# Performance work log

Measured on AMD Instinct MI355X. Metric: run time of the kernel, lower is better.

The kernel has to match this reference:

```python
import jax, jax.numpy as jnp
import numpy as np

HEADS = 2
C1 = 33    # per-head out channels, conv1
C2 = 550   # per-head out channels, conv2


def _lin_params(key, fan_in, fan_out):
    kw, kb = jax.random.split(key)
    scale = 1.0 / np.sqrt(fan_in)
    W = jax.random.uniform(kw, (fan_in, fan_out), jnp.float32, -scale, scale)
    b = jax.random.uniform(kb, (fan_out,), jnp.float32, -scale, scale)
    return W, b


def transformer_conv(x, src, dst, Wq, bq, Wk, bk, Wv, bv, Ws, bs, heads, out_ch):
    """PyG TransformerConv (concat=True, root_weight=True, beta=False)."""
    N = x.shape[0]
    q = (x @ Wq + bq).reshape(N, heads, out_ch)  # query of target node i
    k = (x @ Wk + bk).reshape(N, heads, out_ch)  # key of source node j
    v = (x @ Wv + bv).reshape(N, heads, out_ch)  # value of source node j
    # attention logits per edge: [E, H]
    alpha = jnp.einsum('ehc,ehc->eh', q[dst], k[src]) / jnp.sqrt(jnp.float32(out_ch))
    # segment softmax over incoming edges of each dst node
    m = jax.lax.stop_gradient(jax.ops.segment_max(alpha, dst, num_segments=N))  # [N,H]
    e = jnp.exp(alpha - m[dst])
    denom = jax.ops.segment_sum(e, dst, num_segments=N)  # [N,H]
    a = e / denom[dst]
    # weighted scatter-aggregate of source values: [N,H,C]
    out = jax.ops.segment_sum(a[..., None] * v[src], dst, num_segments=N)
    out = out.reshape(N, heads * out_ch)
    # root/skip connection
    out = out + x @ Ws + bs
    return out


def setup_inputs() -> dict:
    key = jax.random.key(0)
    ks = jax.random.split(key, 10)
    N, E, IN = 20000, 120000, 256
    x = jax.random.normal(ks[0], (N, IN), jnp.float32)
    edge_index = jax.random.randint(ks[1], (2, E), 0, N, jnp.int64 if jax.config.jax_enable_x64 else jnp.int32)
    d = {'x': x, 'edge_index': edge_index}
    # conv1: IN -> heads*C1
    d['Wq1'], d['bq1'] = _lin_params(ks[2], IN, HEADS * C1)
    d['Wk1'], d['bk1'] = _lin_params(ks[3], IN, HEADS * C1)
    d['Wv1'], d['bv1'] = _lin_params(ks[4], IN, HEADS * C1)
    d['Ws1'], d['bs1'] = _lin_params(ks[5], IN, HEADS * C1)
    # conv2: heads*C1 -> heads*C2
    IN2 = HEADS * C1
    d['Wq2'], d['bq2'] = _lin_params(ks[6], IN2, HEADS * C2)
    d['Wk2'], d['bk2'] = _lin_params(ks[7], IN2, HEADS * C2)
    d['Wv2'], d['bv2'] = _lin_params(ks[8], IN2, HEADS * C2)
    d['Ws2'], d['bs2'] = _lin_params(ks[9], IN2, HEADS * C2)
    return d


def reference(x, edge_index, Wq1, bq1, Wk1, bk1, Wv1, bv1, Ws1, bs1,
              Wq2, bq2, Wk2, bk2, Wv2, bv2, Ws2, bs2):
    src, dst = edge_index[0], edge_index[1]
    h = transformer_conv(x, src, dst, Wq1, bq1, Wk1, bk1, Wv1, bv1, Ws1, bs1, HEADS, C1)
    h = transformer_conv(h, src, dst, Wq2, bq2, Wk2, bk2, Wv2, bv2, Ws2, bs2, HEADS, C2)
    # x.view(N, 550, heads).max(dim=2) -- faithful to the original reshape layout
    h = h.reshape(h.shape[0], C2, HEADS)
    return jnp.max(h, axis=2)
```

## Files before the change

### kernel.cpp

```cpp
#include <hip/hip_runtime.h>
#include <math.h>

#define HEADS 2
#define C1    33
#define C2    550
#define D1    66
#define D2    1100
#define IN1   256
#define PROJW 288
#define KU    224
#define N2P   1152
#define KZ    96
#define ZW    144

typedef __attribute__((ext_vector_type(8))) short bfrag;
typedef __attribute__((ext_vector_type(4))) float f32x4;

__device__ inline unsigned short f2bf(float f) {
    unsigned int u = __float_as_uint(f);
    u += 0x7FFFu + ((u >> 16) & 1u);
    return (unsigned short)(u >> 16);
}

__device__ inline int xcd_slot(int bid, int slots) {
    return (bid >> 3) + (bid & 7) * slots;
}

__global__ void k_cvt(const float* __restrict__ x, unsigned short* __restrict__ xb, int total4) {
    int i = blockIdx.x * blockDim.x + threadIdx.x;
    if (i >= total4) return;
    float4 v = ((const float4*)x)[i];
    ushort4 o;
    o.x = f2bf(v.x); o.y = f2bf(v.y); o.z = f2bf(v.z); o.w = f2bf(v.w);
    ((ushort4*)xb)[i] = o;
}

__global__ void k_prep1(const float* __restrict__ Wq, const float* __restrict__ bq,
                        const float* __restrict__ Wk, const float* __restrict__ bk,
                        const float* __restrict__ Wv, const float* __restrict__ bv,
                        const float* __restrict__ Ws, const float* __restrict__ bs,
                        unsigned short* __restrict__ Wt1, float* __restrict__ bcat) {
    int bid = blockIdx.x;
    int lk = bid & 3, t = bid >> 2;
    int ks = t & 7, g = t >> 3;
    int col = threadIdx.x;
    int c = g * 96 + col;
    int k0 = ks * 32 + lk * 8;
    short vals[8];
    float bia = 0.f;
    if (c < 4 * D1) {
        int m = c / D1, j = c % D1;
        const float* W; const float* B;
        switch (m) {
            case 0: W = Wq; B = bq; break;
            case 1: W = Wk; B = bk; break;
            case 2: W = Wv; B = bv; break;
            default: W = Ws; B = bs; break;
        }
        #pragma unroll
        for (int e = 0; e < 8; e++) vals[e] = (short)f2bf(W[(size_t)(k0 + e) * D1 + j]);
        bia = B[j];
    } else {
        #pragma unroll
        for (int e = 0; e < 8; e++) vals[e] = 0;
    }
    *(bfrag*)&Wt1[((size_t)bid * 96 + col) * 8] = *(bfrag*)vals;
    if (ks == 0 && lk == 0) bcat[c] = bia;
}

__global__ void k_prep2(const float* __restrict__ Wv2, const float* __restrict__ bv2,
                        const float* __restrict__ Ws2, const float* __restrict__ bs2,
                        unsigned short* __restrict__ W2t) {
    int bid = blockIdx.x;
    int lk = bid & 3, t = bid >> 2;
    int ks = t % 7, g = t / 7;
    int col = threadIdx.x;
    int c = g * 96 + col;
    int k0 = ks * 32 + lk * 8;
    short vals[8];
    #pragma unroll
    for (int e = 0; e < 8; e++) {
        int k = k0 + e;
        float val = 0.f;
        if (c < D2) {
            if (c < C2) {
                if (k < 66) val = Wv2[(size_t)k * D2 + c];
                else if (k >= 132 && k < 198) val = Ws2[(size_t)(k - 132) * D2 + c];
                else if (k == 198) val = bv2[c];
                else if (k == 223) val = bs2[c];
            } else {
                if (k >= 66 && k < 132) val = Wv2[(size_t)(k - 66) * D2 + c];
                else if (k >= 132 && k < 198) val = Ws2[(size_t)(k - 132) * D2 + c];
                else if (k == 199) val = bv2[c];
                else if (k == 223) val = bs2[c];
            }
        }
        vals[e] = (short)f2bf(val);
    }
    *(bfrag*)&W2t[((size_t)bid * 96 + col) * 8] = *(bfrag*)vals;
}

__global__ void k_hist(const int* __restrict__ dst, int E, int* __restrict__ cnt) {
    int e = blockIdx.x * blockDim.x + threadIdx.x;
    if (e < E) atomicAdd(&cnt[dst[e]], 1);
}

__global__ void k_scan(const int* __restrict__ cnt, int* __restrict__ roff,
                       int* __restrict__ pos, int N) {
    __shared__ int wsum[16];
    __shared__ int carry_s;
    int tid = threadIdx.x, wid = tid >> 6, lane = tid & 63;
    if (tid == 0) { carry_s = 0; roff[0] = 0; }
    __syncthreads();
    for (int base = 0; base < N; base += 1024) {
        int i = base + tid;
        int v = (i < N) ? cnt[i] : 0;
        int x = v;
        #pragma unroll
        for (int s = 1; s < 64; s <<= 1) {
            int t = __shfl_up(x, s, 64);
            if (lane >= s) x += t;
        }
        if (lane == 63) wsum[wid] = x;
        __syncthreads();
        if (tid < 16) {
            int y = wsum[tid];
            #pragma unroll
            for (int s = 1; s < 16; s <<= 1) {
                int t = __shfl_up(y, s, 16);
                if (tid >= s) y += t;
            }
            wsum[tid] = y;
        }
        __syncthreads();
        int carry = carry_s;
        int incl = carry + (wid ? wsum[wid - 1] : 0) + x;
        if (i < N) { roff[i + 1] = incl; pos[i] = incl - v; }
        __syncthreads();
        if (tid == 0) carry_s = carry + wsum[15];
        __syncthreads();
    }
}

__global__ void k_fill(const int* __restrict__ src, const int* __restrict__ dst, int E,
                       int* __restrict__ pos, int* __restrict__ elist) {
    int e = blockIdx.x * blockDim.x + threadIdx.x;
    if (e < E) {
        int slot = atomicAdd(&pos[dst[e]], 1);
        elist[slot] = src[e];
    }
}

__global__ __launch_bounds__(256) void k_mm1(
        const unsigned short* __restrict__ A, const unsigned short* __restrict__ B,
        const float* __restrict__ bias, float* __restrict__ proj, int N,
        int nRow, int slots) {
    int s = xcd_slot(blockIdx.x, slots);
    if (s >= nRow * 3) return;
    int rowt = s / 3, g = s - rowt * 3;
    int cbase = g * 96;
    int wave = threadIdx.x >> 6, lane = threadIdx.x & 63;
    int lr = lane & 15, lk = lane >> 4;
    int rbase = rowt * 128 + wave * 32;
    int ar[2];
    #pragma unroll
    for (int mi = 0; mi < 2; mi++) {
        int r = rbase + mi * 16 + lr;
        ar[mi] = (r < N) ? r : (N - 1);
    }
    bfrag a[2][8];
    #pragma unroll
    for (int mi = 0; mi < 2; mi++)
        #pragma unroll
        for (int ks = 0; ks < 8; ks++)
            a[mi][ks] = *(const bfrag*)(A + (size_t)ar[mi] * IN1 + ks * 32 + lk * 8);
    f32x4 acc[2][6];
    #pragma unroll
    for (int mi = 0; mi < 2; mi++)
        #pragma unroll
        for (int ni = 0; ni < 6; ni++) acc[mi][ni] = (f32x4){0.f, 0.f, 0.f, 0.f};
    #pragma unroll
    for (int ks = 0; ks < 8; ks++) {
        bfrag b[6];
        #pragma unroll
        for (int ni = 0; ni < 6; ni++)
            b[ni] = *(const bfrag*)(B + (size_t)(g * 8 + ks) * 3072 + lk * 768 + (ni * 16 + lr) * 8);
        #pragma unroll
        for (int mi = 0; mi < 2; mi++)
            #pragma unroll
            for (int ni = 0; ni < 6; ni++)
                acc[mi][ni] = __builtin_amdgcn_mfma_f32_16x16x32_bf16(a[mi][ks], b[ni], acc[mi][ni], 0, 0, 0);
    }
    #pragma unroll
    for (int mi = 0; mi < 2; mi++) {
        #pragma unroll
        for (int ni = 0; ni < 6; ni++) {
            int col = cbase + ni * 16 + lr;
            float bia = bias[col];
            #pragma unroll
            for (int r = 0; r < 4; r++) {
                int row = rbase + mi * 16 + lk * 4 + r;
                if (row < N) proj[(size_t)row * PROJW + col] = acc[mi][ni][r] + bia;
            }
        }
    }
}

__global__ __launch_bounds__(128) void k_conv1(
        const float* __restrict__ proj, const int* __restrict__ roff,
        const int* __restrict__ elist, float* __restrict__ h1,
        unsigned short* __restrict__ h1b, int N) {
    int n = blockIdx.x;
    int h = threadIdx.x >> 6;
    int lane = threadIdx.x & 63;
    int half = lane >> 5, l32 = lane & 31;
    size_t pb = (size_t)n * PROJW;
    int hc = h * C1;
    float q_a = proj[pb + hc + l32];
    float q_b = (l32 == 0) ? proj[pb + hc + 32] : 0.f;
    int E0 = roff[n], E1 = roff[n + 1];
    float m = -INFINITY, lsum = 0.f, aca = 0.f, acb = 0.f;
    const float isc = 0.17407765595569785f;
    int i = E0 + half;
    for (; i + 2 < E1; i += 4) {
        int s0 = elist[i], s1 = elist[i + 2];
        size_t b0 = (size_t)s0 * PROJW, b1 = (size_t)s1 * PROJW;
        float k0a = proj[b0 + 66 + hc + l32];
        float k0b = (l32 == 0) ? proj[b0 + 66 + hc + 32] : 0.f;
        float k1a = proj[b1 + 66 + hc + l32];
        float k1b = (l32 == 0) ? proj[b1 + 66 + hc + 32] : 0.f;
        float v0a = proj[b0 + 132 + hc + l32];
        float v0b = (l32 == 0) ? proj[b0 + 132 + hc + 32] : 0.f;
        float v1a = proj[b1 + 132 + hc + l32];
        float v1b = (l32 == 0) ? proj[b1 + 132 + hc + 32] : 0.f;
        float p0 = q_a * k0a + q_b * k0b;
        float p1 = q_a * k1a + q_b * k1b;
        #pragma unroll
        for (int off = 16; off >= 1; off >>= 1) {
            p0 += __shfl_xor(p0, off, 32);
            p1 += __shfl_xor(p1, off, 32);
        }
        float a0 = p0 * isc, a1 = p1 * isc;
        float mp = fmaxf(a0, a1);
        float e0 = __expf(a0 - mp), e1 = __expf(a1 - mp);
        float lp = e0 + e1;
        float apa = e0 * v0a + e1 * v1a;
        float apb = e0 * v0b + e1 * v1b;
        float mnew = fmaxf(m, mp);
        float sc = __expf(m - mnew), sp = __expf(mp - mnew);
        lsum = lsum * sc + lp * sp;
        aca = aca * sc + apa * sp;
        acb = acb * sc + apb * sp;
        m = mnew;
    }
    for (; i < E1; i += 2) {
        int s = elist[i];
        size_t sb = (size_t)s * PROJW;
        float ka = proj[sb + 66 + hc + l32];
        float kb = (l32 == 0) ? proj[sb + 66 + hc + 32] : 0.f;
        float va = proj[sb + 132 + hc + l32];
        float vb = (l32 == 0) ? proj[sb + 132 + hc + 32] : 0.f;
        float p = q_a * ka + q_b * kb;
        #pragma unroll
        for (int off = 16; off >= 1; off >>= 1) p += __shfl_xor(p, off, 32);
        float alpha = p * isc;
        float mnew = fmaxf(m, alpha);
        float sc = __expf(m - mnew);
        float pe = __expf(alpha - mnew);
        lsum = lsum * sc + pe;
        aca = aca * sc + pe * va;
        acb = acb * sc + pe * vb;
        m = mnew;
    }
    float mO  = __shfl_xor(m, 32, 64);
    float lO  = __shfl_xor(lsum, 32, 64);
    float aaO = __shfl_xor(aca, 32, 64);
    float abO = __shfl_xor(acb, 32, 64);
    float mnew = fmaxf(m, mO);
    float sS = (m  > -INFINITY) ? __expf(m  - mnew) : 0.f;
    float sO = (mO > -INFINITY) ? __expf(mO - mnew) : 0.f;
    lsum = lsum * sS + lO * sO;
    aca  = aca * sS + aaO * sO;
    acb  = acb * sS + abO * sO;
    float inv = (lsum > 0.f) ? 1.f / lsum : 0.f;
    if (half == 0) {
        float s1a = proj[pb + 198 + hc + l32];
        float val = aca * inv + s1a;
        h1[(size_t)n * D1 + hc + l32] = val;
        h1b[(size_t)n * KZ + hc + l32] = f2bf(val);
        if (l32 == 0) {
            float s1b = proj[pb + 198 + hc + 32];
            float valb = acb * inv + s1b;
            h1[(size_t)n * D1 + hc + 32] = valb;
            h1b[(size_t)n * KZ + hc + 32] = f2bf(valb);
        }
    } else if (h == 1 && l32 < 30) {
        h1b[(size_t)n * KZ + D1 + l32] = 0;
    }
}

__global__ __launch_bounds__(256) void k_precomp(
        const float* __restrict__ Wq2, const float* __restrict__ bq2,
        const float* __restrict__ Wk2, const float* __restrict__ bk2,
        float* __restrict__ G, float* __restrict__ wqbk,
        float* __restrict__ wkbq, float* __restrict__ cc) {
    int wave = threadIdx.x >> 6, lane = threadIdx.x & 63;
    int j = blockIdx.x * 4 + wave;
    if (j >= 8978) return;
    const float *u, *v;
    float* outp;
    if (j < 8976) {
        int h = j / 4488;
        int r = j % 4488;
        int a = r / 68, b = r % 68;
        if (b < 66)      { u = Wq2 + (size_t)a * D2 + h * C2; v = Wk2 + (size_t)b * D2 + h * C2; outp = &G[h * 4356 + a * 66 + b]; }
        else if (b == 66){ u = Wq2 + (size_t)a * D2 + h * C2; v = bk2 + h * C2;                  outp = &wqbk[h * 66 + a]; }
        else             { u = Wk2 + (size_t)a * D2 + h * C2; v = bq2 + h * C2;                  outp = &wkbq[h * 66 + a]; }
    } else {
        int h = j - 8976;
        u = bq2 + h * C2; v = bk2 + h * C2; outp = &cc[h];
    }
    float acc = 0.f;
    for (int c = lane; c < C2; c += 64) acc += u[c] * v[c];
    #pragma unroll
    for (int off = 32; off >= 1; off >>= 1) acc += __shfl_xor(acc, off, 64);
    if (lane == 0) *outp = acc;
}

__global__ void k_prepz(const float* __restrict__ G, const float* __restrict__ wqbk,
                        const float* __restrict__ wkbq, unsigned short* __restrict__ GBt) {
    int bid = blockIdx.x;
    int lk = bid & 3, t = bid >> 2;
    int ks = t % 3, g = t / 3;
    int col = threadIdx.x;
    int r = g * 96 + col;
    int k0 = ks * 32 + lk * 8;
    short vals[8];
    #pragma unroll
    for (int e = 0; e < 8; e++) {
        int k = k0 + e;
        float v = 0.f;
        if (k < D1) {
            if (r < 132) v = G[r * D1 + k];
            else if (r < 134) v = wqbk[(r - 132) * D1 + k];
            else if (r < 136) v = wkbq[(r - 134) * D1 + k];
        }
        vals[e] = (short)f2bf(v);
    }
    *(bfrag*)&GBt[((size_t)bid * 96 + col) * 8] = *(bfrag*)vals;
}

__global__ __launch_bounds__(256) void k_mmz(
        const unsigned short* __restrict__ A, const unsigned short* __restrict__ B,
        float* __restrict__ Z, int N, int nRow, int slots) {
    int s = xcd_slot(blockIdx.x, slots);
    if (s >= nRow * 2) return;
    int rowt = s >> 1, g = s & 1;
    int wave = threadIdx.x >> 6, lane = threadIdx.x & 63;
    int lr = lane & 15, lk = lane >> 4;
    int rbase = rowt * 64 + (wave >> 1) * 32;
    int ch = (wave & 1) * 48;
    int cbase = g * 96 + ch;
    f32x4 acc[2][3];
    #pragma unroll
    for (int i = 0; i < 2; i++)
        #pragma unroll
        for (int j = 0; j < 3; j++) acc[i][j] = (f32x4){0.f, 0.f, 0.f, 0.f};
    int ar[2];
    #pragma unroll
    for (int mi = 0; mi < 2; mi++) {
        int r = rbase + mi * 16 + lr;
        ar[mi] = (r < N) ? r : (N - 1);
    }
    #pragma unroll
    for (int ks = 0; ks < 3; ks++) {
        bfrag a[2], b[3];
        #pragma unroll
        for (int mi = 0; mi < 2; mi++)
            a[mi] = *(const bfrag*)(A + (size_t)ar[mi] * KZ + ks * 32 + lk * 8);
        #pragma unroll
        for (int ni = 0; ni < 3; ni++)
            b[ni] = *(const bfrag*)(B + (size_t)(g * 3 + ks) * 3072 + lk * 768 + (ch + ni * 16 + lr) * 8);
        #pragma unroll
        for (int mi = 0; mi < 2; mi++)
            #pragma unroll
            for (int ni = 0; ni < 3; ni++)
                acc[mi][ni] = __builtin_amdgcn_mfma_f32_16x16x32_bf16(a[mi], b[ni], acc[mi][ni], 0, 0, 0);
    }
    #pragma unroll
    for (int mi = 0; mi < 2; mi++) {
        #pragma unroll
        for (int ni = 0; ni < 3; ni++) {
            int col = cbase + ni * 16 + lr;
            if (col >= 136) continue;
            #pragma unroll
            for (int r = 0; r < 4; r++) {
                int row = rbase + mi * 16 + lk * 4 + r;
                if (row < N) Z[(size_t)row * ZW + col] = acc[mi][ni][r];
            }
        }
    }
}

__global__ __launch_bounds__(128) void k_conv2(
        const float* __restrict__ h1, const float* __restrict__ Z,
        const float* __restrict__ cc, const int* __restrict__ roff,
        const int* __restrict__ elist, unsigned short* __restrict__ U, int N) {
    int n = blockIdx.x;
    int h = threadIdx.x >> 6;
    int lane = threadIdx.x & 63;
    int half = lane >> 5, l32 = lane & 31;
    int hD = h * D1;
    size_t nb = (size_t)n * D1;
    float hd_a = h1[nb + l32];
    float hd_b = h1[nb + 32 + l32];
    float hd_c = (l32 < 2) ? h1[nb + 64 + l32] : 0.f;
    float adv = Z[(size_t)n * ZW + 132 + h] + cc[h];
    int E0 = roff[n], E1 = roff[n + 1];
    float m = -INFINITY, lsum = 0.f, aa = 0.f, ab = 0.f, ac = 0.f;
    const float isc = 0.04264014327112209f;
    int i = E0 + half;
    for (; i + 2 < E1; i += 4) {
        int s0 = elist[i], s1 = elist[i + 2];
        const float* z0 = Z + (size_t)s0 * ZW;
        const float* z1 = Z + (size_t)s1 * ZW;
        float z0c = (l32 < 2) ? z0[hD + 64 + l32] : 0.f;
        float z1c = (l32 < 2) ? z1[hD + 64 + l32] : 0.f;
        float p0 = hd_a * z0[hD + l32] + hd_b * z0[hD + 32 + l32] + hd_c * z0c;
        float p1 = hd_a * z1[hD + l32] + hd_b * z1[hD + 32 + l32] + hd_c * z1c;
        float as0 = z0[134 + h], as1 = z1[134 + h];
        #pragma unroll
        for (int off = 16; off >= 1; off >>= 1) {
            p0 += __shfl_xor(p0, off, 32);
            p1 += __shfl_xor(p1, off, 32);
        }
        float al0 = (p0 + adv + as0) * isc;
        float al1 = (p1 + adv + as1) * isc;
        size_t v0b = (size_t)s0 * D1, v1b = (size_t)s1 * D1;
        float v0a = h1[v0b + l32], v0bb = h1[v0b + 32 + l32];
        float v0c = (l32 < 2) ? h1[v0b + 64 + l32] : 0.f;
        float v1a = h1[v1b + l32], v1bb = h1[v1b + 32 + l32];
        float v1c = (l32 < 2) ? h1[v1b + 64 + l32] : 0.f;
        float mp = fmaxf(al0, al1);
        float e0 = __expf(al0 - mp), e1 = __expf(al1 - mp);
        float lp = e0 + e1;
        float mnew = fmaxf(m, mp);
        float sc = __expf(m - mnew), sp = __expf(mp - mnew);
        lsum = lsum * sc + lp * sp;
        aa = aa * sc + (e0 * v0a + e1 * v1a) * sp;
        ab = ab * sc + (e0 * v0bb + e1 * v1bb) * sp;
        ac = ac * sc + (e0 * v0c + e1 * v1c) * sp;
        m = mnew;
    }
    for (; i < E1; i += 2) {
        int s = elist[i];
        const float* zr = Z + (size_t)s * ZW;
        float zc = (l32 < 2) ? zr[hD + 64 + l32] : 0.f;
        float p = hd_a * zr[hD + l32] + hd_b * zr[hD + 32 + l32] + hd_c * zc;
        float as_ = zr[134 + h];
        #pragma unroll
        for (int off = 16; off >= 1; off >>= 1) p += __shfl_xor(p, off, 32);
        float alpha = (p + adv + as_) * isc;
        size_t vb = (size_t)s * D1;
        float va = h1[vb + l32], vbb = h1[vb + 32 + l32];
        float vc = (l32 < 2) ? h1[vb + 64 + l32] : 0.f;
        float mnew = fmaxf(m, alpha);
        float sc = __expf(m - mnew);
        float pe = __expf(alpha - mnew);
        lsum = lsum * sc + pe;
        aa = aa * sc + pe * va;
        ab = ab * sc + pe * vbb;
        ac = ac * sc + pe * vc;
        m = mnew;
    }
    float mO  = __shfl_xor(m, 32, 64);
    float lO  = __shfl_xor(lsum, 32, 64);
    float aaO = __shfl_xor(aa, 32, 64);
    float abO = __shfl_xor(ab, 32, 64);
    float acO = __shfl_xor(ac, 32, 64);
    float mnew = fmaxf(m, mO);
    float sS = (m  > -INFINITY) ? __expf(m  - mnew) : 0.f;
    float sO = (mO > -INFINITY) ? __expf(mO - mnew) : 0.f;
    lsum = lsum * sS + lO * sO;
    aa = aa * sS + aaO * sO;
    ab = ab * sS + abO * sO;
    ac = ac * sS + acO * sO;
    float inv = (lsum > 0.f) ? 1.f / lsum : 0.f;
    size_t ub = (size_t)n * KU;
    if (half == 0) {
        U[ub + hD + l32] = f2bf(aa * inv);
        if (l32 < 2) U[ub + hD + 64 + l32] = f2bf(ac * inv);
    } else {
        U[ub + hD + 32 + l32] = f2bf(ab * inv);
    }
    if (lane == 0) U[ub + 198 + h] = (lsum > 0.f) ? (unsigned short)0x3F80 : (unsigned short)0;
    if (h == 0) {
        if (half == 0) {
            U[ub + 132 + l32] = f2bf(hd_a);
            if (l32 < 2) U[ub + 132 + 64 + l32] = f2bf(hd_c);
            if (l32 == 2) U[ub + 223] = (unsigned short)0x3F80;
        } else {
            U[ub + 132 + 32 + l32] = f2bf(hd_b);
        }
    } else if (half == 1 && l32 < 23) {
        U[ub + 200 + l32] = 0;
    }
}

__global__ __launch_bounds__(256) void k_mm2(
        const unsigned short* __restrict__ A, const unsigned short* __restrict__ B,
        float* __restrict__ out, int N, int nRow, int slots) {
    __shared__ float ot[4][32][49];
    int s = xcd_slot(blockIdx.x, slots);
    if (s >= nRow * 12) return;
    int rowt = s / 12, g = s - rowt * 12;
    int wave = threadIdx.x >> 6, lane = threadIdx.x & 63;
    int lr = lane & 15, lk = lane >> 4;
    int rbase = rowt * 128 + wave * 32;
    int ar[2];
    #pragma unroll
    for (int mi = 0; mi < 2; mi++) {
        int r = rbase + mi * 16 + lr;
        ar[mi] = (r < N) ? r : (N - 1);
    }
    bfrag a[2][7];
    #pragma unroll
    for (int mi = 0; mi < 2; mi++)
        #pragma unroll
        for (int ks = 0; ks < 7; ks++)
            a[mi][ks] = *(const bfrag*)(A + (size_t)ar[mi] * KU + ks * 32 + lk * 8);
    f32x4 acc[2][6];
    #pragma unroll
    for (int mi = 0; mi < 2; mi++)
        #pragma unroll
        for (int ni = 0; ni < 6; ni++) acc[mi][ni] = (f32x4){0.f, 0.f, 0.f, 0.f};
    #pragma unroll
    for (int ks = 0; ks < 7; ks++) {
        bfrag b[6];
        #pragma unroll
        for (int ni = 0; ni < 6; ni++)
            b[ni] = *(const bfrag*)(B + (size_t)(g * 7 + ks) * 3072 + lk * 768 + (ni * 16 + lr) * 8);
        #pragma unroll
        for (int mi = 0; mi < 2; mi++)
            #pragma unroll
            for (int ni = 0; ni < 6; ni++)
                acc[mi][ni] = __builtin_amdgcn_mfma_f32_16x16x32_bf16(a[mi][ks], b[ni], acc[mi][ni], 0, 0, 0);
    }
    #pragma unroll
    for (int mi = 0; mi < 2; mi++) {
        #pragma unroll
        for (int ni = 0; ni < 6; ni++) {
            #pragma unroll
            for (int r = 0; r < 4; r++) {
                float val = acc[mi][ni][r];
                float oth = __shfl_xor(val, 1, 64);
                if (!(lane & 1))
                    ot[wave][mi * 16 + lk * 4 + r][ni * 8 + (lr >> 1)] = fmaxf(val, oth);
            }
        }
    }
    __syncthreads();
    int colb = g * 48;
    #pragma unroll
    for (int i = 0; i < 24; i++) {
        int t = i * 64 + lane;
        int r32 = t / 48, pos = t - r32 * 48;
        int row = rbase + r32;
        int col = colb + pos;
        if (row < N && col < C2)
            out[(size_t)row * C2 + col] = ot[wave][r32][pos];
    }
}

extern "C" void kernel_launch(void* const* d_in, const int* in_sizes, int n_in,
                              void* d_out, int out_size, void* d_ws, size_t ws_size,
                              hipStream_t stream) {
    const float* x  = (const float*)d_in[0];
    const int*   ei = (const int*)d_in[1];
    int N = in_sizes[0] / IN1;
    int E = in_sizes[1] / 2;
    const int* src = ei;
    const int* dst = ei + E;

    const float *Wq1 = (const float*)d_in[2],  *bq1 = (const float*)d_in[3];
    const float *Wk1 = (const float*)d_in[4],  *bk1 = (const float*)d_in[5];
    const float *Wv1 = (const float*)d_in[6],  *bv1 = (const float*)d_in[7];
    const float *Ws1 = (const float*)d_in[8],  *bs1 = (const float*)d_in[9];
    const float *Wq2 = (const float*)d_in[10], *bq2 = (const float*)d_in[11];
    const float *Wk2 = (const float*)d_in[12], *bk2 = (const float*)d_in[13];
    const float *Wv2 = (const float*)d_in[14], *bv2 = (const float*)d_in[15];
    const float *Ws2 = (const float*)d_in[16], *bs2 = (const float*)d_in[17];

    char* w = (char*)d_ws;
    size_t off = 0;
    auto take = [&](size_t bytes) { size_t o = off; off = (off + bytes + 255) & ~(size_t)255; return o; };

    unsigned short* xb = (unsigned short*)(w + take((size_t)N * IN1 * 2));
    size_t proj_off = take((size_t)N * PROJW * 4);
    float* proj = (float*)(w + proj_off);
    float* Z = proj;
    unsigned short* U = (unsigned short*)(w + proj_off + (size_t)N * ZW * 4);
    float* h1   = (float*)(w + take((size_t)N * D1 * 4));
    unsigned short* h1b = (unsigned short*)(w + take((size_t)N * KZ * 2));
    float* G    = (float*)(w + take((size_t)2 * D1 * D1 * 4));
    float* wqbk = (float*)(w + take(2 * D1 * 4));
    float* wkbq = (float*)(w + take(2 * D1 * 4));
    float* cc   = (float*)(w + take(2 * 4));
    unsigned short* GBt = (unsigned short*)(w + take((size_t)24 * 96 * 8 * 2));
    unsigned short* Wt1 = (unsigned short*)(w + take((size_t)96 * 96 * 8 * 2));
    float* bcat = (float*)(w + take(PROJW * 4));
    unsigned short* W2t = (unsigned short*)(w + take((size_t)336 * 96 * 8 * 2));
    int* cnt   = (int*)(w + take((size_t)N * 4));
    int* roff  = (int*)(w + take((size_t)(N + 1) * 4));
    int* pos   = (int*)(w + take((size_t)N * 4));
    int* elist = (int*)(w + take((size_t)E * 4));

    hipMemsetAsync(cnt, 0, (size_t)N * sizeof(int), stream);
    k_hist<<<(E + 255) / 256, 256, 0, stream>>>(dst, E, cnt);
    k_scan<<<1, 1024, 0, stream>>>(cnt, roff, pos, N);
    k_fill<<<(E + 255) / 256, 256, 0, stream>>>(src, dst, E, pos, elist);

    k_cvt<<<(N * IN1 / 4 + 255) / 256, 256, 0, stream>>>(x, xb, N * IN1 / 4);
    k_prep1<<<96, 96, 0, stream>>>(Wq1, bq1, Wk1, bk1, Wv1, bv1, Ws1, bs1, Wt1, bcat);
    k_prep2<<<336, 96, 0, stream>>>(Wv2, bv2, Ws2, bs2, W2t);
    k_precomp<<<(8978 + 3) / 4, 256, 0, stream>>>(Wq2, bq2, Wk2, bk2, G, wqbk, wkbq, cc);
    k_prepz<<<24, 96, 0, stream>>>(G, wqbk, wkbq, GBt);

    int nRow1 = (N + 127) / 128;
    int tot1  = nRow1 * 3;
    int slots1 = (tot1 + 7) / 8;
    int nRowZ = (N + 63) / 64;
    int totZ  = nRowZ * 2;
    int slotsZ = (totZ + 7) / 8;
    int nRow2 = (N + 127) / 128;
    int tot2  = nRow2 * 12;
    int slots2 = (tot2 + 7) / 8;

    k_mm1<<<slots1 * 8, 256, 0, stream>>>(xb, Wt1, bcat, proj, N, nRow1, slots1);
    k_conv1<<<N, 128, 0, stream>>>(proj, roff, elist, h1, h1b, N);

    k_mmz<<<slotsZ * 8, 256, 0, stream>>>(h1b, GBt, Z, N, nRowZ, slotsZ);

    k_conv2<<<N, 128, 0, stream>>>(h1, Z, cc, roff, elist, U, N);

    k_mm2<<<slots2 * 8, 256, 0, stream>>>(U, W2t, (float*)d_out, N, nRow2, slots2);
}
```

Before: 173.1 us.

## Store intermediates in bf16, fuse x conversion into mm1, merge precompute kernels

```diff
diff --git a/kernel.cpp b/kernel.cpp
--- a/kernel.cpp
+++ b/kernel.cpp
@@ -9,7 +9,6 @@
 #define IN1   256
 #define PROJW 288
 #define KU    224
-#define N2P   1152
 #define KZ    96
 #define ZW    144
 
@@ -21,18 +20,12 @@
     u += 0x7FFFu + ((u >> 16) & 1u);
     return (unsigned short)(u >> 16);
 }
+__device__ inline float bf2f(unsigned short u) {
+    return __uint_as_float((unsigned int)u << 16);
+}
 
 __device__ inline int xcd_slot(int bid, int slots) {
     return (bid >> 3) + (bid & 7) * slots;
-}
-
-__global__ void k_cvt(const float* __restrict__ x, unsigned short* __restrict__ xb, int total4) {
-    int i = blockIdx.x * blockDim.x + threadIdx.x;
-    if (i >= total4) return;
-    float4 v = ((const float4*)x)[i];
-    ushort4 o;
-    o.x = f2bf(v.x); o.y = f2bf(v.y); o.z = f2bf(v.z); o.w = f2bf(v.w);
-    ((ushort4*)xb)[i] = o;
 }
 
 __global__ void k_prep1(const float* __restrict__ Wq, const float* __restrict__ bq,
@@ -151,9 +144,48 @@
     }
 }
 
+__global__ __launch_bounds__(256) void k_precomp(
+        const float* __restrict__ Wq2, const float* __restrict__ bq2,
+        const float* __restrict__ Wk2, const float* __restrict__ bk2,
+        unsigned short* __restrict__ GBt, float* __restrict__ cc) {
+    int wave = threadIdx.x >> 6, lane = threadIdx.x & 63;
+    int j = blockIdx.x * 4 + wave;
+    if (j >= 8978) return;
+    const float *u, *v;
+    int h = 0, a = 0, b = 0;
+    if (j < 8976) {
+        h = j / 4488;
+        int r = j % 4488;
+        a = r / 68; b = r % 68;
+        if (b < 66)      { u = Wq2 + (size_t)a * D2 + h * C2; v = Wk2 + (size_t)b * D2 + h * C2; }
+        else if (b == 66){ u = Wq2 + (size_t)a * D2 + h * C2; v = bk2 + h * C2; }
+        else             { u = Wk2 + (size_t)a * D2 + h * C2; v = bq2 + h * C2; }
+    } else {
+        h = j - 8976;
+        u = bq2 + h * C2; v = bk2 + h * C2;
+    }
+    float acc = 0.f;
+    for (int c = lane; c < C2; c += 64) acc += u[c] * v[c];
+    #pragma unroll
+    for (int off = 32; off >= 1; off >>= 1) acc += __shfl_xor(acc, off, 64);
+    if (lane == 0) {
+        if (j < 8976) {
+            int r, k;
+            if (b < 66)      { r = h * 66 + a; k = b; }
+            else if (b == 66){ r = 132 + h;    k = a; }
+            else             { r = 134 + h;    k = a; }
+            int g = r / 96, cm = r % 96;
+            int ks2 = k >> 5, rem = k & 31, lk2 = rem >> 3, e = rem & 7;
+            GBt[(((size_t)(g * 3 + ks2) * 4 + lk2) * 96 + cm) * 8 + e] = f2bf(acc);
+        } else {
+            cc[h] = acc;
+        }
+    }
+}
+
 __global__ __launch_bounds__(256) void k_mm1(
-        const unsigned short* __restrict__ A, const unsigned short* __restrict__ B,
-        const float* __restrict__ bias, float* __restrict__ proj, int N,
+        const float* __restrict__ X, const unsigned short* __restrict__ B,
+        const float* __restrict__ bias, unsigned short* __restrict__ projb, int N,
         int nRow, int slots) {
     int s = xcd_slot(blockIdx.x, slots);
     if (s >= nRow * 3) return;
@@ -172,8 +204,17 @@
     #pragma unroll
     for (int mi = 0; mi < 2; mi++)
         #pragma unroll
-        for (int ks = 0; ks < 8; ks++)
-            a[mi][ks] = *(const bfrag*)(A + (size_t)ar[mi] * IN1 + ks * 32 + lk * 8);
+        for (int ks = 0; ks < 8; ks++) {
+            const float* p = X + (size_t)ar[mi] * IN1 + ks * 32 + lk * 8;
+            float4 v0 = *(const float4*)p;
+            float4 v1 = *(const float4*)(p + 4);
+            bfrag r;
+            r[0] = (short)f2bf(v0.x); r[1] = (short)f2bf(v0.y);
+            r[2] = (short)f2bf(v0.z); r[3] = (short)f2bf(v0.w);
+            r[4] = (short)f2bf(v1.x); r[5] = (short)f2bf(v1.y);
+            r[6] = (short)f2bf(v1.z); r[7] = (short)f2bf(v1.w);
+            a[mi][ks] = r;
+        }
     f32x4 acc[2][6];
     #pragma unroll
     for (int mi = 0; mi < 2; mi++)
@@ -200,24 +241,23 @@
             #pragma unroll
             for (int r = 0; r < 4; r++) {
                 int row = rbase + mi * 16 + lk * 4 + r;
-                if (row < N) proj[(size_t)row * PROJW + col] = acc[mi][ni][r] + bia;
+                if (row < N) projb[(size_t)row * PROJW + col] = f2bf(acc[mi][ni][r] + bia);
             }
         }
     }
 }
 
 __global__ __launch_bounds__(128) void k_conv1(
-        const float* __restrict__ proj, const int* __restrict__ roff,
-        const int* __restrict__ elist, float* __restrict__ h1,
-        unsigned short* __restrict__ h1b, int N) {
+        const unsigned short* __restrict__ projb, const int* __restrict__ roff,
+        const int* __restrict__ elist, unsigned short* __restrict__ h1b, int N) {
     int n = blockIdx.x;
     int h = threadIdx.x >> 6;
     int lane = threadIdx.x & 63;
     int half = lane >> 5, l32 = lane & 31;
     size_t pb = (size_t)n * PROJW;
     int hc = h * C1;
-    float q_a = proj[pb + hc + l32];
-    float q_b = (l32 == 0) ? proj[pb + hc + 32] : 0.f;
+    float q_a = bf2f(projb[pb + hc + l32]);
+    float q_b = (l32 == 0) ? bf2f(projb[pb + hc + 32]) : 0.f;
     int E0 = roff[n], E1 = roff[n + 1];
     float m = -INFINITY, lsum = 0.f, aca = 0.f, acb = 0.f;
     const float isc = 0.17407765595569785f;
@@ -225,14 +265,14 @@
     for (; i + 2 < E1; i += 4) {
         int s0 = elist[i], s1 = elist[i + 2];
         size_t b0 = (size_t)s0 * PROJW, b1 = (size_t)s1 * PROJW;
-        float k0a = proj[b0 + 66 + hc + l32];
-        float k0b = (l32 == 0) ? proj[b0 + 66 + hc + 32] : 0.f;
-        float k1a = proj[b1 + 66 + hc + l32];
-        float k1b = (l32 == 0) ? proj[b1 + 66 + hc + 32] : 0.f;
-        float v0a = proj[b0 + 132 + hc + l32];
-        float v0b = (l32 == 0) ? proj[b0 + 132 + hc + 32] : 0.f;
-        float v1a = proj[b1 + 132 + hc + l32];
-        float v1b = (l32 == 0) ? proj[b1 + 132 + hc + 32] : 0.f;
+        float k0a = bf2f(projb[b0 + 66 + hc + l32]);
+        float k0b = (l32 == 0) ? bf2f(projb[b0 + 66 + hc + 32]) : 0.f;
+        float k1a = bf2f(projb[b1 + 66 + hc + l32]);
+        float k1b = (l32 == 0) ? bf2f(projb[b1 + 66 + hc + 32]) : 0.f;
+        float v0a = bf2f(projb[b0 + 132 + hc + l32]);
+        float v0b = (l32 == 0) ? bf2f(projb[b0 + 132 + hc + 32]) : 0.f;
+        float v1a = bf2f(projb[b1 + 132 + hc + l32]);
+        float v1b = (l32 == 0) ? bf2f(projb[b1 + 132 + hc + 32]) : 0.f;
         float p0 = q_a * k0a + q_b * k0b;
         float p1 = q_a * k1a + q_b * k1b;
         #pragma unroll
@@ -256,10 +296,10 @@
     for (; i < E1; i += 2) {
         int s = elist[i];
         size_t sb = (size_t)s * PROJW;
-        float ka = proj[sb + 66 + hc + l32];
-        float kb = (l32 == 0) ? proj[sb + 66 + hc + 32] : 0.f;
-        float va = proj[sb + 132 + hc + l32];
-        float vb = (l32 == 0) ? proj[sb + 132 + hc + 32] : 0.f;
+        float ka = bf2f(projb[sb + 66 + hc + l32]);
+        float kb = (l32 == 0) ? bf2f(projb[sb + 66 + hc + 32]) : 0.f;
+        float va = bf2f(projb[sb + 132 + hc + l32]);
+        float vb = (l32 == 0) ? bf2f(projb[sb + 132 + hc + 32]) : 0.f;
         float p = q_a * ka + q_b * kb;
         #pragma unroll
         for (int off = 16; off >= 1; off >>= 1) p += __shfl_xor(p, off, 32);
@@ -284,14 +324,12 @@
     acb  = acb * sS + abO * sO;
     float inv = (lsum > 0.f) ? 1.f / lsum : 0.f;
     if (half == 0) {
-        float s1a = proj[pb + 198 + hc + l32];
+        float s1a = bf2f(projb[pb + 198 + hc + l32]);
         float val = aca * inv + s1a;
-        h1[(size_t)n * D1 + hc + l32] = val;
         h1b[(size_t)n * KZ + hc + l32] = f2bf(val);
         if (l32 == 0) {
-            float s1b = proj[pb + 198 + hc + 32];
+            float s1b = bf2f(projb[pb + 198 + hc + 32]);
             float valb = acb * inv + s1b;
-            h1[(size_t)n * D1 + hc + 32] = valb;
             h1b[(size_t)n * KZ + hc + 32] = f2bf(valb);
         }
     } else if (h == 1 && l32 < 30) {
@@ -299,60 +337,9 @@
     }
 }
 
-__global__ __launch_bounds__(256) void k_precomp(
-        const float* __restrict__ Wq2, const float* __restrict__ bq2,
-        const float* __restrict__ Wk2, const float* __restrict__ bk2,
-        float* __restrict__ G, float* __restrict__ wqbk,
-        float* __restrict__ wkbq, float* __restrict__ cc) {
-    int wave = threadIdx.x >> 6, lane = threadIdx.x & 63;
-    int j = blockIdx.x * 4 + wave;
-    if (j >= 8978) return;
-    const float *u, *v;
-    float* outp;
-    if (j < 8976) {
-        int h = j / 4488;
-        int r = j % 4488;
-        int a = r / 68, b = r % 68;
-        if (b < 66)      { u = Wq2 + (size_t)a * D2 + h * C2; v = Wk2 + (size_t)b * D2 + h * C2; outp = &G[h * 4356 + a * 66 + b]; }
-        else if (b == 66){ u = Wq2 + (size_t)a * D2 + h * C2; v = bk2 + h * C2;                  outp = &wqbk[h * 66 + a]; }
-        else             { u = Wk2 + (size_t)a * D2 + h * C2; v = bq2 + h * C2;                  outp = &wkbq[h * 66 + a]; }
-    } else {
-        int h = j - 8976;
-        u = bq2 + h * C2; v = bk2 + h * C2; outp = &cc[h];
-    }
-    float acc = 0.f;
-    for (int c = lane; c < C2; c += 64) acc += u[c] * v[c];
-    #pragma unroll
-    for (int off = 32; off >= 1; off >>= 1) acc += __shfl_xor(acc, off, 64);
-    if (lane == 0) *outp = acc;
-}
-
-__global__ void k_prepz(const float* __restrict__ G, const float* __restrict__ wqbk,
-                        const float* __restrict__ wkbq, unsigned short* __restrict__ GBt) {
-    int bid = blockIdx.x;
-    int lk = bid & 3, t = bid >> 2;
-    int ks = t % 3, g = t / 3;
-    int col = threadIdx.x;
-    int r = g * 96 + col;
-    int k0 = ks * 32 + lk * 8;
-    short vals[8];
-    #pragma unroll
-    for (int e = 0; e < 8; e++) {
-        int k = k0 + e;
-        float v = 0.f;
-        if (k < D1) {
-            if (r < 132) v = G[r * D1 + k];
-            else if (r < 134) v = wqbk[(r - 132) * D1 + k];
-            else if (r < 136) v = wkbq[(r - 134) * D1 + k];
-        }
-        vals[e] = (short)f2bf(v);
-    }
-    *(bfrag*)&GBt[((size_t)bid * 96 + col) * 8] = *(bfrag*)vals;
-}
-
 __global__ __launch_bounds__(256) void k_mmz(
         const unsigned short* __restrict__ A, const unsigned short* __restrict__ B,
-        float* __restrict__ Z, int N, int nRow, int slots) {
+        unsigned short* __restrict__ Zb, int N, int nRow, int slots) {
     int s = xcd_slot(blockIdx.x, slots);
     if (s >= nRow * 2) return;
     int rowt = s >> 1, g = s & 1;
@@ -396,14 +383,14 @@
             #pragma unroll
             for (int r = 0; r < 4; r++) {
                 int row = rbase + mi * 16 + lk * 4 + r;
-                if (row < N) Z[(size_t)row * ZW + col] = acc[mi][ni][r];
+                if (row < N) Zb[(size_t)row * ZW + col] = f2bf(acc[mi][ni][r]);
             }
         }
     }
 }
 
 __global__ __launch_bounds__(128) void k_conv2(
-        const float* __restrict__ h1, const float* __restrict__ Z,
+        const unsigned short* __restrict__ h1b, const unsigned short* __restrict__ Zb,
         const float* __restrict__ cc, const int* __restrict__ roff,
         const int* __restrict__ elist, unsigned short* __restrict__ U, int N) {
     int n = blockIdx.x;
@@ -411,24 +398,24 @@
     int lane = threadIdx.x & 63;
     int half = lane >> 5, l32 = lane & 31;
     int hD = h * D1;
-    size_t nb = (size_t)n * D1;
-    float hd_a = h1[nb + l32];
-    float hd_b = h1[nb + 32 + l32];
-    float hd_c = (l32 < 2) ? h1[nb + 64 + l32] : 0.f;
-    float adv = Z[(size_t)n * ZW + 132 + h] + cc[h];
+    size_t nb = (size_t)n * KZ;
+    float hd_a = bf2f(h1b[nb + l32]);
+    float hd_b = bf2f(h1b[nb + 32 + l32]);
+    float hd_c = (l32 < 2) ? bf2f(h1b[nb + 64 + l32]) : 0.f;
+    float adv = bf2f(Zb[(size_t)n * ZW + 132 + h]) + cc[h];
     int E0 = roff[n], E1 = roff[n + 1];
     float m = -INFINITY, lsum = 0.f, aa = 0.f, ab = 0.f, ac = 0.f;
     const float isc = 0.04264014327112209f;
     int i = E0 + half;
     for (; i + 2 < E1; i += 4) {
         int s0 = elist[i], s1 = elist[i + 2];
-        const float* z0 = Z + (size_t)s0 * ZW;
-        const float* z1 = Z + (size_t)s1 * ZW;
-        float z0c = (l32 < 2) ? z0[hD + 64 + l32] : 0.f;
-        float z1c = (l32 < 2) ? z1[hD + 64 + l32] : 0.f;
-        float p0 = hd_a * z0[hD + l32] + hd_b * z0[hD + 32 + l32] + hd_c * z0c;
-        float p1 = hd_a * z1[hD + l32] + hd_b * z1[hD + 32 + l32] + hd_c * z1c;
-        float as0 = z0[134 + h], as1 = z1[134 + h];
+        const unsigned short* z0 = Zb + (size_t)s0 * ZW;
+        const unsigned short* z1 = Zb + (size_t)s1 * ZW;
+        float z0c = (l32 < 2) ? bf2f(z0[hD + 64 + l32]) : 0.f;
+        float z1c = (l32 < 2) ? bf2f(z1[hD + 64 + l32]) : 0.f;
+        float p0 = hd_a * bf2f(z0[hD + l32]) + hd_b * bf2f(z0[hD + 32 + l32]) + hd_c * z0c;
+        float p1 = hd_a * bf2f(z1[hD + l32]) + hd_b * bf2f(z1[hD + 32 + l32]) + hd_c * z1c;
+        float as0 = bf2f(z0[134 + h]), as1 = bf2f(z1[134 + h]);
         #pragma unroll
         for (int off = 16; off >= 1; off >>= 1) {
             p0 += __shfl_xor(p0, off, 32);
@@ -436,11 +423,11 @@
         }
         float al0 = (p0 + adv + as0) * isc;
         float al1 = (p1 + adv + as1) * isc;
-        size_t v0b = (size_t)s0 * D1, v1b = (size_t)s1 * D1;
-        float v0a = h1[v0b + l32], v0bb = h1[v0b + 32 + l32];
-        float v0c = (l32 < 2) ? h1[v0b + 64 + l32] : 0.f;
-        float v1a = h1[v1b + l32], v1bb = h1[v1b + 32 + l32];
-        float v1c = (l32 < 2) ? h1[v1b + 64 + l32] : 0.f;
+        size_t v0b = (size_t)s0 * KZ, v1b = (size_t)s1 * KZ;
+        float v0a = bf2f(h1b[v0b + l32]), v0bb = bf2f(h1b[v0b + 32 + l32]);
+        float v0c = (l32 < 2) ? bf2f(h1b[v0b + 64 + l32]) : 0.f;
+        float v1a = bf2f(h1b[v1b + l32]), v1bb = bf2f(h1b[v1b + 32 + l32]);
+        float v1c = (l32 < 2) ? bf2f(h1b[v1b + 64 + l32]) : 0.f;
         float mp = fmaxf(al0, al1);
         float e0 = __expf(al0 - mp), e1 = __expf(al1 - mp);
         float lp = e0 + e1;
@@ -454,16 +441,16 @@
     }
     for (; i < E1; i += 2) {
         int s = elist[i];
-        const float* zr = Z + (size_t)s * ZW;
-        float zc = (l32 < 2) ? zr[hD + 64 + l32] : 0.f;
-        float p = hd_a * zr[hD + l32] + hd_b * zr[hD + 32 + l32] + hd_c * zc;
-        float as_ = zr[134 + h];
+        const unsigned short* zr = Zb + (size_t)s * ZW;
+        float zc = (l32 < 2) ? bf2f(zr[hD + 64 + l32]) : 0.f;
+        float p = hd_a * bf2f(zr[hD + l32]) + hd_b * bf2f(zr[hD + 32 + l32]) + hd_c * zc;
+        float as_ = bf2f(zr[134 + h]);
         #pragma unroll
         for (int off = 16; off >= 1; off >>= 1) p += __shfl_xor(p, off, 32);
         float alpha = (p + adv + as_) * isc;
-        size_t vb = (size_t)s * D1;
-        float va = h1[vb + l32], vbb = h1[vb + 32 + l32];
-        float vc = (l32 < 2) ? h1[vb + 64 + l32] : 0.f;
+        size_t vb = (size_t)s * KZ;
+        float va = bf2f(h1b[vb + l32]), vbb = bf2f(h1b[vb + 32 + l32]);
+        float vc = (l32 < 2) ? bf2f(h1b[vb + 64 + l32]) : 0.f;
         float mnew = fmaxf(m, alpha);
         float sc = __expf(m - mnew);
         float pe = __expf(alpha - mnew);
@@ -595,16 +582,10 @@
     size_t off = 0;
     auto take = [&](size_t bytes) { size_t o = off; off = (off + bytes + 255) & ~(size_t)255; return o; };
 
-    unsigned short* xb = (unsigned short*)(w + take((size_t)N * IN1 * 2));
-    size_t proj_off = take((size_t)N * PROJW * 4);
-    float* proj = (float*)(w + proj_off);
-    float* Z = proj;
-    unsigned short* U = (unsigned short*)(w + proj_off + (size_t)N * ZW * 4);
-    float* h1   = (float*)(w + take((size_t)N * D1 * 4));
-    unsigned short* h1b = (unsigned short*)(w + take((size_t)N * KZ * 2));
-    float* G    = (float*)(w + take((size_t)2 * D1 * D1 * 4));
-    float* wqbk = (float*)(w + take(2 * D1 * 4));
-    float* wkbq = (float*)(w + take(2 * D1 * 4));
+    unsigned short* projb = (unsigned short*)(w + take((size_t)N * PROJW * 2));
+    unsigned short* Zb    = (unsigned short*)(w + take((size_t)N * ZW * 2));
+    unsigned short* U     = (unsigned short*)(w + take((size_t)N * KU * 2));
+    unsigned short* h1b   = (unsigned short*)(w + take((size_t)N * KZ * 2));
     float* cc   = (float*)(w + take(2 * 4));
     unsigned short* GBt = (unsigned short*)(w + take((size_t)24 * 96 * 8 * 2));
     unsigned short* Wt1 = (unsigned short*)(w + take((size_t)96 * 96 * 8 * 2));
@@ -620,11 +601,9 @@
     k_scan<<<1, 1024, 0, stream>>>(cnt, roff, pos, N);
     k_fill<<<(E + 255) / 256, 256, 0, stream>>>(src, dst, E, pos, elist);
 
-    k_cvt<<<(N * IN1 / 4 + 255) / 256, 256, 0, stream>>>(x, xb, N * IN1 / 4);
     k_prep1<<<96, 96, 0, stream>>>(Wq1, bq1, Wk1, bk1, Wv1, bv1, Ws1, bs1, Wt1, bcat);
     k_prep2<<<336, 96, 0, stream>>>(Wv2, bv2, Ws2, bs2, W2t);
-    k_precomp<<<(8978 + 3) / 4, 256, 0, stream>>>(Wq2, bq2, Wk2, bk2, G, wqbk, wkbq, cc);
-    k_prepz<<<24, 96, 0, stream>>>(G, wqbk, wkbq, GBt);
+    k_precomp<<<(8978 + 3) / 4, 256, 0, stream>>>(Wq2, bq2, Wk2, bk2, GBt, cc);
 
     int nRow1 = (N + 127) / 128;
     int tot1  = nRow1 * 3;
@@ -636,12 +615,12 @@
     int tot2  = nRow2 * 12;
     int slots2 = (tot2 + 7) / 8;
 
-    k_mm1<<<slots1 * 8, 256, 0, stream>>>(xb, Wt1, bcat, proj, N, nRow1, slots1);
-    k_conv1<<<N, 128, 0, stream>>>(proj, roff, elist, h1, h1b, N);
-
-    k_mmz<<<slotsZ * 8, 256, 0, stream>>>(h1b, GBt, Z, N, nRowZ, slotsZ);
-
-    k_conv2<<<N, 128, 0, stream>>>(h1, Z, cc, roff, elist, U, N);
+    k_mm1<<<slots1 * 8, 256, 0, stream>>>(x, Wt1, bcat, projb, N, nRow1, slots1);
+    k_conv1<<<N, 128, 0, stream>>>(projb, roff, elist, h1b, N);
+
+    k_mmz<<<slotsZ * 8, 256, 0, stream>>>(h1b, GBt, Zb, N, nRowZ, slotsZ);
+
+    k_conv2<<<N, 128, 0, stream>>>(h1b, Zb, cc, roff, elist, U, N);
 
     k_mm2<<<slots2 * 8, 256, 0, stream>>>(U, W2t, (float*)d_out, N, nRow2, slots2);
 }
```

Result: slower. 177.1 us (+2.3%).
